# Optimization experiments

Hardware: AMD Instinct MI355X
Metric: run time of the kernel (lower is better)

Reference implementation:

```python
import jax, jax.numpy as jnp
import numpy as np

B, N, D, W = 4, 4096, 256, 7
K = 2 * W + 1  # 15 taps: positions [i-2w, ..., i]
H = 4 * D
EPS = 1e-5


def layer_norm(x, g, b):
    mu = jnp.mean(x, axis=-1, keepdims=True)
    var = jnp.mean(jnp.square(x - mu), axis=-1, keepdims=True)
    return (x - mu) * jax.lax.rsqrt(var + EPS) * g + b


def setup_inputs() -> dict:
    key = jax.random.key(0)
    ks = jax.random.split(key, 8)
    s = 0.02
    return {
        "x": jax.random.normal(ks[0], (B, N, D), dtype=jnp.float32),
        # w_mix[k] is the DxD block of the (K*D -> D) Linear acting on offset k-2w
        "w_mix": (jax.random.normal(ks[1], (K, D, D), dtype=jnp.float32) * s),
        "b_mix": jnp.zeros((D,), dtype=jnp.float32),
        "g1": jnp.ones((D,), jnp.float32) + 0.1 * jax.random.normal(ks[2], (D,), jnp.float32),
        "b1": 0.1 * jax.random.normal(ks[3], (D,), jnp.float32),
        "w_ff1": jax.random.normal(ks[4], (D, H), dtype=jnp.float32) * s,
        "b_ff1": jnp.zeros((H,), dtype=jnp.float32),
        "w_ff2": jax.random.normal(ks[5], (H, D), dtype=jnp.float32) * s,
        "b_ff2": jnp.zeros((D,), dtype=jnp.float32),
        "g2": jnp.ones((D,), jnp.float32) + 0.1 * jax.random.normal(ks[6], (D,), jnp.float32),
        "b2": 0.1 * jax.random.normal(ks[7], (D,), jnp.float32),
    }


def reference(x, w_mix, b_mix, g1, b1, w_ff1, b_ff1, w_ff2, b_ff2, g2, b2):
    # Causal windowed concat + Linear == causal 1D conv with kernel K=2w+1.
    # torch feats chunk k holds x[i - 2w + k]; conv tap k with left pad 2w
    # sees exactly x[i - 2w + k], so kernel = mix weight reshaped (K, D, D).
    mix = jax.lax.conv_general_dilated(
        x, w_mix, window_strides=(1,), padding=[(2 * W, 0)],
        dimension_numbers=("NWC", "WIO", "NWC"),
    ) + b_mix  # [B, N, D]
    # Dropout is identity in eval mode (reference baseline).
    h = layer_norm(x + mix, g1, b1)
    ff = jnp.dot(jax.nn.gelu(jnp.dot(h, w_ff1) + b_ff1, approximate=False), w_ff2) + b_ff2
    return layer_norm(h + ff, g2, b2)
```

## Files before the change

### kernel.cpp

```cpp
#include <hip/hip_runtime.h>
#include <cstdint>

#define DD     256
#define HH     1024
#define NNSEQ  4096
#define KDIM   3840
#define MT     64
#define XROWS  78
#define XPITCH 264
#define APITCH 520
#define FPITCH 260
#define EPSLN  1e-5f

typedef unsigned short u16;
typedef __attribute__((ext_vector_type(8))) short short8;
typedef __attribute__((ext_vector_type(4))) float f32x4;

#define MFMA(a, b, c) __builtin_amdgcn_mfma_f32_16x16x32_bf16(a, b, c, 0, 0, 0)

__device__ __forceinline__ u16 f2bf(float f) {
  unsigned u = __float_as_uint(f);
  u += 0x7FFF + ((u >> 16) & 1);
  return (u16)(u >> 16);
}
__device__ __forceinline__ float bf2f(u16 s) { return __uint_as_float(((unsigned)s) << 16); }

__global__ __launch_bounds__(256) void k_prep(
    const float* __restrict__ wmix, const float* __restrict__ wff1,
    const float* __restrict__ wff2, u16* __restrict__ wpk,
    u16* __restrict__ w1pk, u16* __restrict__ w2pk)
{
  __shared__ float t[32][257];
  const int b = blockIdx.x, tid = threadIdx.x;

  u16* dst;
  if (b < 120) {
    dst = wpk + (size_t)b * 8192;
    for (int r = 0; r < 32; ++r)
      t[r][tid] = wmix[(size_t)(b * 32 + r) * 256 + tid];
  } else if (b < 152) {
    const int u = b - 120, c2 = u >> 3, s = u & 7;
    dst = w1pk + (size_t)u * 8192;
    for (int r = 0; r < 32; ++r)
      t[r][tid] = wff1[(size_t)(s * 32 + r) * 1024 + c2 * 256 + tid];
  } else {
    const int u = b - 152, c2 = u >> 3, s = u & 7;
    dst = w2pk + (size_t)u * 8192;
    for (int r = 0; r < 32; ++r)
      t[r][tid] = wff2[(size_t)(c2 * 256 + s * 32 + r) * 256 + tid];
  }
  __syncthreads();

  const int l = tid & 63, q = l >> 4, cl = l & 15;
#pragma unroll
  for (int f = 0; f < 4; ++f) {
    const int fi = f * 4 + (tid >> 6);
    const int n = fi * 16 + cl;
    uint4 pk;
    unsigned* p = (unsigned*)&pk;
#pragma unroll
    for (int jj = 0; jj < 4; ++jj)
      p[jj] = (unsigned)f2bf(t[q * 8 + jj * 2][n]) | ((unsigned)f2bf(t[q * 8 + jj * 2 + 1][n]) << 16);
    *(uint4*)&dst[(size_t)fi * 512 + l * 8] = pk;
  }
}

__global__ __launch_bounds__(512) void k_conv(
    const float* __restrict__ x, const u16* __restrict__ wpk,
    const float* __restrict__ bmix, u16* __restrict__ yb)
{
  __shared__ u16 xs[XROWS * XPITCH];

  const int tid = threadIdx.x;
  const int wv = tid >> 6, l = tid & 63, q = l >> 4, cl = l & 15;
  const int mg = wv >> 2, ng = wv & 3;
  const int mtile = blockIdx.x >> 2, nb = blockIdx.x & 3;
  const long tok0 = (long)mtile * MT;
  const int n0 = (int)(tok0 & (NNSEQ - 1));

  {
    const int cslot = (tid & 63) * 4;
    for (int r = tid >> 6; r < XROWS; r += 8) {
      const int nloc = n0 - 14 + r;
      float4 v = make_float4(0.f, 0.f, 0.f, 0.f);
      if (nloc >= 0) v = *(const float4*)&x[(tok0 - 14 + r) * DD + cslot];
      uint2 pk;
      pk.x = (unsigned)f2bf(v.x) | ((unsigned)f2bf(v.y) << 16);
      pk.y = (unsigned)f2bf(v.z) | ((unsigned)f2bf(v.w) << 16);
      *(uint2*)&xs[r * XPITCH + cslot] = pk;
    }
  }
  __syncthreads();

  f32x4 acc[4];
  {
    const float bm = (mg == 0) ? bmix[nb * 64 + ng * 16 + cl] : 0.f;
#pragma unroll
    for (int mt = 0; mt < 4; ++mt) acc[mt] = (f32x4){bm, bm, bm, bm};
  }

  const u16* bbase = wpk + (size_t)(mg * 60) * 8192 + (size_t)(nb * 4 + ng) * 512 + (size_t)l * 8;

#define LOAD_A(dst, s_)                                                         \
  {                                                                             \
    const int ks = mg * 60 + (s_);                                              \
    const int xrow = ks >> 3, c0 = (ks & 7) * 32;                               \
    _Pragma("unroll")                                                           \
    for (int mt = 0; mt < 4; ++mt)                                              \
      dst[mt] = *(const short8*)&xs[(xrow + mt * 16 + cl) * XPITCH + c0 + q * 8]; \
  }
#define LOAD_B(dst, s_) dst = *(const short8*)(bbase + (size_t)(s_) * 8192);

  {
    short8 af[4][4], bfr[4];
    LOAD_A(af[0], 0) LOAD_B(bfr[0], 0)
    LOAD_A(af[1], 1) LOAD_B(bfr[1], 1)
    LOAD_A(af[2], 2) LOAD_B(bfr[2], 2)
    LOAD_A(af[3], 3) LOAD_B(bfr[3], 3)

#pragma unroll 4
    for (int s = 0; s < 60; ++s) {
      const int cur = s & 3;
#pragma unroll
      for (int mt = 0; mt < 4; ++mt)
        acc[mt] = MFMA(af[cur][mt], bfr[cur], acc[mt]);
      if (s + 4 < 60) {
        LOAD_A(af[cur], s + 4)
        LOAD_B(bfr[cur], s + 4)
      }
    }
  }
#undef LOAD_A
#undef LOAD_B

  __syncthreads();
  float* rbuf = (float*)xs;
  if (mg == 1) {
#pragma unroll
    for (int mt = 0; mt < 4; ++mt)
#pragma unroll
      for (int reg = 0; reg < 4; ++reg)
        rbuf[(mt * 16 + q * 4 + reg) * 65 + ng * 16 + cl] = acc[mt][reg];
  }
  __syncthreads();

  if (mg == 0) {
#pragma unroll
    for (int mt = 0; mt < 4; ++mt)
#pragma unroll
      for (int reg = 0; reg < 4; ++reg) {
        const int row = mt * 16 + q * 4 + reg;
        const int col = nb * 64 + ng * 16 + cl;
        const float y = acc[mt][reg] + rbuf[row * 65 + ng * 16 + cl]
                      + x[(tok0 + row) * DD + col];
        yb[(tok0 + row) * DD + col] = f2bf(y);
      }
  }
}

__global__ __launch_bounds__(512) void k_ffn(
    const u16* __restrict__ yb, const float* __restrict__ g1,
    const float* __restrict__ b1, const u16* __restrict__ w1pk,
    const float* __restrict__ bf1, const u16* __restrict__ w2pk,
    const float* __restrict__ bf2, const float* __restrict__ g2,
    const float* __restrict__ b2, float* __restrict__ out)
{
  __shared__ u16 hs[64 * XPITCH];
  __shared__ u16 asb[64 * APITCH];
  __shared__ float redS[4][64], redS2[4][64];
  __shared__ float muL[64], invL[64];

  const int tid = threadIdx.x;
  const int wv = tid >> 6, l = tid & 63, q = l >> 4, cl = l & 15;
  const int mg = wv >> 2, ng = wv & 3;
  const long tok0 = (long)blockIdx.x * MT;

  {
    const int chunk = tid & 31;
#pragma unroll
    for (int i = 0; i < 4; ++i) {
      const int row = (tid >> 5) + i * 16;
      *(uint4*)&hs[row * XPITCH + chunk * 8] = *(const uint4*)&yb[(tok0 + row) * DD + chunk * 8];
    }
  }
  __syncthreads();

  {
    const int row = tid >> 3, seg = tid & 7;
    uint4 v[4];
#pragma unroll
    for (int i = 0; i < 4; ++i)
      v[i] = *(const uint4*)&hs[row * XPITCH + seg * 32 + i * 8];
    float yv[32];
#pragma unroll
    for (int i = 0; i < 4; ++i) {
      const unsigned* w = (const unsigned*)&v[i];
#pragma unroll
      for (int j = 0; j < 4; ++j) {
        yv[i * 8 + j * 2]     = __uint_as_float(w[j] << 16);
        yv[i * 8 + j * 2 + 1] = __uint_as_float(w[j] & 0xffff0000u);
      }
    }
    float s = 0.f, s2 = 0.f;
#pragma unroll
    for (int k = 0; k < 32; ++k) { s += yv[k]; s2 += yv[k] * yv[k]; }
#pragma unroll
    for (int off = 1; off < 8; off <<= 1) { s += __shfl_xor(s, off, 64); s2 += __shfl_xor(s2, off, 64); }
    const float mu  = s * (1.f / DD);
    const float var = s2 * (1.f / DD) - mu * mu;
    const float inv = rsqrtf(var + EPSLN);
#pragma unroll
    for (int i = 0; i < 4; ++i) {
      const float4 gv0 = *(const float4*)&g1[seg * 32 + i * 8];
      const float4 gv1 = *(const float4*)&g1[seg * 32 + i * 8 + 4];
      const float4 bv0 = *(const float4*)&b1[seg * 32 + i * 8];
      const float4 bv1 = *(const float4*)&b1[seg * 32 + i * 8 + 4];
      const float g[8] = {gv0.x, gv0.y, gv0.z, gv0.w, gv1.x, gv1.y, gv1.z, gv1.w};
      const float bb[8] = {bv0.x, bv0.y, bv0.z, bv0.w, bv1.x, bv1.y, bv1.z, bv1.w};
      uint4 pk;
      unsigned* p = (unsigned*)&pk;
#pragma unroll
      for (int j = 0; j < 4; ++j) {
        const float h0 = (yv[i * 8 + j * 2]     - mu) * inv * g[j * 2]     + bb[j * 2];
        const float h1 = (yv[i * 8 + j * 2 + 1] - mu) * inv * g[j * 2 + 1] + bb[j * 2 + 1];
        p[j] = (unsigned)f2bf(h0) | ((unsigned)f2bf(h1) << 16);
      }
      *(uint4*)&hs[row * XPITCH + seg * 32 + i * 8] = pk;
    }
  }
  __syncthreads();

  f32x4 acc2[4][4];
#pragma unroll
  for (int nt = 0; nt < 4; ++nt) {
    const float bv = (mg == 0) ? bf2[ng * 64 + nt * 16 + cl] : 0.f;
#pragma unroll
    for (int mt = 0; mt < 4; ++mt) acc2[mt][nt] = (f32x4){bv, bv, bv, bv};
  }

  for (int c = 0; c < 2; ++c) {
    f32x4 acc1[4][4];
#pragma unroll
    for (int nt = 0; nt < 4; ++nt) {
      const float bv = bf1[c * 512 + wv * 64 + nt * 16 + cl];
#pragma unroll
      for (int mt = 0; mt < 4; ++mt) acc1[mt][nt] = (f32x4){bv, bv, bv, bv};
    }
#pragma unroll
    for (int s = 0; s < 8; ++s) {
      short8 a[4], b[4];
#pragma unroll
      for (int mt = 0; mt < 4; ++mt)
        a[mt] = *(const short8*)&hs[(mt * 16 + cl) * XPITCH + s * 32 + q * 8];
      const u16* bp = w1pk + (size_t)((c * 2 + mg) * 8 + s) * 8192 + (size_t)(ng * 4) * 512 + (size_t)l * 8;
#pragma unroll
      for (int nt = 0; nt < 4; ++nt)
        b[nt] = *(const short8*)(bp + nt * 512);
#pragma unroll
      for (int mt = 0; mt < 4; ++mt)
#pragma unroll
        for (int nt = 0; nt < 4; ++nt)
          acc1[mt][nt] = MFMA(a[mt], b[nt], acc1[mt][nt]);
    }
#pragma unroll
    for (int mt = 0; mt < 4; ++mt)
#pragma unroll
      for (int nt = 0; nt < 4; ++nt)
#pragma unroll
        for (int reg = 0; reg < 4; ++reg) {
          const float v = acc1[mt][nt][reg];
          const float g = 0.5f * v * (1.f + erff(v * 0.70710678118654752f));
          asb[(mt * 16 + q * 4 + reg) * APITCH + wv * 64 + nt * 16 + cl] = f2bf(g);
        }
    __syncthreads();
#pragma unroll
    for (int s = 0; s < 8; ++s) {
      short8 a[4], b[4];
#pragma unroll
      for (int mt = 0; mt < 4; ++mt)
        a[mt] = *(const short8*)&asb[(mt * 16 + cl) * APITCH + mg * 256 + s * 32 + q * 8];
      const u16* bp = w2pk + (size_t)((c * 2 + mg) * 8 + s) * 8192 + (size_t)(ng * 4) * 512 + (size_t)l * 8;
#pragma unroll
      for (int nt = 0; nt < 4; ++nt)
        b[nt] = *(const short8*)(bp + nt * 512);
#pragma unroll
      for (int mt = 0; mt < 4; ++mt)
#pragma unroll
        for (int nt = 0; nt < 4; ++nt)
          acc2[mt][nt] = MFMA(a[mt], b[nt], acc2[mt][nt]);
    }
    __syncthreads();
  }

  float* fbuf = (float*)asb;
  if (mg == 1) {
#pragma unroll
    for (int mt = 0; mt < 4; ++mt)
#pragma unroll
      for (int nt = 0; nt < 4; ++nt)
#pragma unroll
        for (int reg = 0; reg < 4; ++reg)
          fbuf[(mt * 16 + q * 4 + reg) * FPITCH + ng * 64 + nt * 16 + cl] = acc2[mt][nt][reg];
  }
  __syncthreads();

  if (mg == 0) {
    float ps[4][4], ps2[4][4];
#pragma unroll
    for (int mt = 0; mt < 4; ++mt)
#pragma unroll
      for (int reg = 0; reg < 4; ++reg) {
        const int row = mt * 16 + q * 4 + reg;
        float s = 0.f, s2 = 0.f;
#pragma unroll
        for (int nt = 0; nt < 4; ++nt) {
          const int col = ng * 64 + nt * 16 + cl;
          float y = acc2[mt][nt][reg] + fbuf[row * FPITCH + col] + bf2f(hs[row * XPITCH + col]);
          acc2[mt][nt][reg] = y;
          s += y; s2 += y * y;
        }
#pragma unroll
        for (int off = 1; off < 16; off <<= 1) { s += __shfl_xor(s, off, 64); s2 += __shfl_xor(s2, off, 64); }
        ps[mt][reg] = s; ps2[mt][reg] = s2;
      }
    if (cl == 0) {
#pragma unroll
      for (int mt = 0; mt < 4; ++mt)
#pragma unroll
        for (int reg = 0; reg < 4; ++reg) {
          const int row = mt * 16 + q * 4 + reg;
          redS[ng][row] = ps[mt][reg]; redS2[ng][row] = ps2[mt][reg];
        }
    }
  }
  __syncthreads();
  if (tid < 64) {
    const float s  = redS[0][tid] + redS[1][tid] + redS[2][tid] + redS[3][tid];
    const float s2 = redS2[0][tid] + redS2[1][tid] + redS2[2][tid] + redS2[3][tid];
    const float mu = s * (1.f / DD);
    const float var = s2 * (1.f / DD) - mu * mu;
    muL[tid] = mu; invL[tid] = rsqrtf(var + EPSLN);
  }
  __syncthreads();

  if (mg == 0) {
#pragma unroll
    for (int nt = 0; nt < 4; ++nt) {
      const int col = ng * 64 + nt * 16 + cl;
      const float gv = g2[col], bv = b2[col];
#pragma unroll
      for (int mt = 0; mt < 4; ++mt)
#pragma unroll
        for (int reg = 0; reg < 4; ++reg) {
          const int row = mt * 16 + q * 4 + reg;
          out[(tok0 + row) * DD + col] = (acc2[mt][nt][reg] - muL[row]) * invL[row] * gv + bv;
        }
    }
  }
}

extern "C" void kernel_launch(void* const* d_in, const int* in_sizes, int n_in,
                              void* d_out, int out_size, void* d_ws, size_t ws_size,
                              hipStream_t stream) {
  const float* x    = (const float*)d_in[0];
  const float* wmix = (const float*)d_in[1];
  const float* bmix = (const float*)d_in[2];
  const float* g1   = (const float*)d_in[3];
  const float* b1   = (const float*)d_in[4];
  const float* wff1 = (const float*)d_in[5];
  const float* bff1 = (const float*)d_in[6];
  const float* wff2 = (const float*)d_in[7];
  const float* bff2 = (const float*)d_in[8];
  const float* g2   = (const float*)d_in[9];
  const float* b2   = (const float*)d_in[10];
  float* out = (float*)d_out;

  u16* wpk  = (u16*)d_ws;
  u16* w1pk = wpk + 983040;
  u16* w2pk = w1pk + 262144;
  u16* yb   = w2pk + 262144;

  k_prep<<<184, 256, 0, stream>>>(wmix, wff1, wff2, wpk, w1pk, w2pk);

  k_conv<<<1024, 512, 0, stream>>>(x, wpk, bmix, yb);
  k_ffn <<<256, 512, 0, stream>>>(yb, g1, b1, w1pk, bff1, w2pk, bff2, g2, b2, out);
}
```

Baseline: 165.6 us.

## Restructure conv and FFN warp tiling to cut split-K reductions and boost reuse

The conv kernel drops from 512 to 256 threads. Each wave now computes a full 64x64 output tile over a quarter of the K dimension, so each loaded A fragment is reused across 4 N-tiles. The split-K partial sums are then combined through a staged tree reduction in shared memory. The FFN kernel changes from a split-K over wave groups to an M-split (each half of the waves owns 32 rows over the full hidden dimension in 4 chunks), which removes the final cross-group reduction buffer and shrinks the activation buffer. This trades fewer redundant loads and reductions for more accumulator registers per wave and more sync stages.

Result: slower. 179.2 us (+8.2%).

```diff
diff --git a/kernel.cpp b/kernel.cpp
--- a/kernel.cpp
+++ b/kernel.cpp
@@ -8,8 +8,6 @@
 #define MT     64
 #define XROWS  78
 #define XPITCH 264
-#define APITCH 520
-#define FPITCH 260
 #define EPSLN  1e-5f
 
 typedef unsigned short u16;
@@ -65,22 +63,22 @@
   }
 }
 
-__global__ __launch_bounds__(512) void k_conv(
+__global__ __launch_bounds__(256, 3) void k_conv(
     const float* __restrict__ x, const u16* __restrict__ wpk,
     const float* __restrict__ bmix, u16* __restrict__ yb)
 {
-  __shared__ u16 xs[XROWS * XPITCH];
+  __shared__ char smem[49920];
+  u16* xs = (u16*)smem;
 
   const int tid = threadIdx.x;
   const int wv = tid >> 6, l = tid & 63, q = l >> 4, cl = l & 15;
-  const int mg = wv >> 2, ng = wv & 3;
   const int mtile = blockIdx.x >> 2, nb = blockIdx.x & 3;
   const long tok0 = (long)mtile * MT;
   const int n0 = (int)(tok0 & (NNSEQ - 1));
 
   {
     const int cslot = (tid & 63) * 4;
-    for (int r = tid >> 6; r < XROWS; r += 8) {
+    for (int r = tid >> 6; r < XROWS; r += 4) {
       const int nloc = n0 - 14 + r;
       float4 v = make_float4(0.f, 0.f, 0.f, 0.f);
       if (nloc >= 0) v = *(const float4*)&x[(tok0 - 14 + r) * DD + cslot];
@@ -92,41 +90,48 @@
   }
   __syncthreads();
 
-  f32x4 acc[4];
-  {
-    const float bm = (mg == 0) ? bmix[nb * 64 + ng * 16 + cl] : 0.f;
-#pragma unroll
-    for (int mt = 0; mt < 4; ++mt) acc[mt] = (f32x4){bm, bm, bm, bm};
-  }
-
-  const u16* bbase = wpk + (size_t)(mg * 60) * 8192 + (size_t)(nb * 4 + ng) * 512 + (size_t)l * 8;
+  f32x4 acc[4][4];
+#pragma unroll
+  for (int nt = 0; nt < 4; ++nt) {
+    const float bm = (wv == 0) ? bmix[nb * 64 + nt * 16 + cl] : 0.f;
+#pragma unroll
+    for (int mt = 0; mt < 4; ++mt) acc[mt][nt] = (f32x4){bm, bm, bm, bm};
+  }
+
+  const u16* bbase = wpk + (size_t)(wv * 30) * 8192 + (size_t)(nb * 4) * 512 + (size_t)l * 8;
 
 #define LOAD_A(dst, s_)                                                         \
   {                                                                             \
-    const int ks = mg * 60 + (s_);                                              \
+    const int ks = wv * 30 + (s_);                                              \
     const int xrow = ks >> 3, c0 = (ks & 7) * 32;                               \
     _Pragma("unroll")                                                           \
     for (int mt = 0; mt < 4; ++mt)                                              \
       dst[mt] = *(const short8*)&xs[(xrow + mt * 16 + cl) * XPITCH + c0 + q * 8]; \
   }
-#define LOAD_B(dst, s_) dst = *(const short8*)(bbase + (size_t)(s_) * 8192);
-
-  {
-    short8 af[4][4], bfr[4];
+#define LOAD_B(dst, s_)                                                         \
+  {                                                                             \
+    const u16* bp = bbase + (size_t)(s_) * 8192;                                \
+    _Pragma("unroll")                                                           \
+    for (int nt = 0; nt < 4; ++nt)                                              \
+      dst[nt] = *(const short8*)(bp + nt * 512);                                \
+  }
+
+  {
+    short8 af[2][4], bfr[2][4];
     LOAD_A(af[0], 0) LOAD_B(bfr[0], 0)
     LOAD_A(af[1], 1) LOAD_B(bfr[1], 1)
-    LOAD_A(af[2], 2) LOAD_B(bfr[2], 2)
-    LOAD_A(af[3], 3) LOAD_B(bfr[3], 3)
-
-#pragma unroll 4
-    for (int s = 0; s < 60; ++s) {
-      const int cur = s & 3;
+
+#pragma unroll 2
+    for (int s = 0; s < 30; ++s) {
+      const int cur = s & 1;
 #pragma unroll
       for (int mt = 0; mt < 4; ++mt)
-        acc[mt] = MFMA(af[cur][mt], bfr[cur], acc[mt]);
-      if (s + 4 < 60) {
-        LOAD_A(af[cur], s + 4)
-        LOAD_B(bfr[cur], s + 4)
+#pragma unroll
+        for (int nt = 0; nt < 4; ++nt)
+          acc[mt][nt] = MFMA(af[cur][mt], bfr[cur][nt], acc[mt][nt]);
+      if (s + 2 < 30) {
+        LOAD_A(af[cur], s + 2)
+        LOAD_B(bfr[cur], s + 2)
       }
     }
   }
@@ -134,28 +139,45 @@
 #undef LOAD_B
 
   __syncthreads();
-  float* rbuf = (float*)xs;
-  if (mg == 1) {
+  float* fb = (float*)smem;
+#define SLOT_W(si)                                                              \
+  _Pragma("unroll")                                                             \
+  for (int mt = 0; mt < 4; ++mt)                                                \
+    _Pragma("unroll")                                                           \
+    for (int nt = 0; nt < 4; ++nt)                                              \
+      _Pragma("unroll")                                                         \
+      for (int reg = 0; reg < 4; ++reg)                                         \
+        fb[(si) * 4160 + (mt * 16 + q * 4 + reg) * 65 + nt * 16 + cl] = acc[mt][nt][reg];
+#define SLOT_R(si)                                                              \
+  _Pragma("unroll")                                                             \
+  for (int mt = 0; mt < 4; ++mt)                                                \
+    _Pragma("unroll")                                                           \
+    for (int nt = 0; nt < 4; ++nt)                                              \
+      _Pragma("unroll")                                                         \
+      for (int reg = 0; reg < 4; ++reg)                                         \
+        acc[mt][nt][reg] += fb[(si) * 4160 + (mt * 16 + q * 4 + reg) * 65 + nt * 16 + cl];
+
+  if (wv == 2) { SLOT_W(0) } else if (wv == 3) { SLOT_W(1) }
+  __syncthreads();
+  if (wv == 0) { SLOT_R(0) } else if (wv == 1) { SLOT_R(1) SLOT_W(2) }
+  __syncthreads();
+  if (wv == 0) {
+    SLOT_R(2)
 #pragma unroll
     for (int mt = 0; mt < 4; ++mt)
 #pragma unroll
-      for (int reg = 0; reg < 4; ++reg)
-        rbuf[(mt * 16 + q * 4 + reg) * 65 + ng * 16 + cl] = acc[mt][reg];
-  }
-  __syncthreads();
-
-  if (mg == 0) {
-#pragma unroll
-    for (int mt = 0; mt < 4; ++mt)
-#pragma unroll
-      for (int reg = 0; reg < 4; ++reg) {
-        const int row = mt * 16 + q * 4 + reg;
-        const int col = nb * 64 + ng * 16 + cl;
-        const float y = acc[mt][reg] + rbuf[row * 65 + ng * 16 + cl]
-                      + x[(tok0 + row) * DD + col];
-        yb[(tok0 + row) * DD + col] = f2bf(y);
-      }
-  }
+      for (int nt = 0; nt < 4; ++nt) {
+        const int col = nb * 64 + nt * 16 + cl;
+#pragma unroll
+        for (int reg = 0; reg < 4; ++reg) {
+          const int row = mt * 16 + q * 4 + reg;
+          const float y = acc[mt][nt][reg] + x[(tok0 + row) * DD + col];
+          yb[(tok0 + row) * DD + col] = f2bf(y);
+        }
+      }
+  }
+#undef SLOT_W
+#undef SLOT_R
 }
 
 __global__ __launch_bounds__(512) void k_ffn(
@@ -166,13 +188,13 @@
     const float* __restrict__ b2, float* __restrict__ out)
 {
   __shared__ u16 hs[64 * XPITCH];
-  __shared__ u16 asb[64 * APITCH];
+  __shared__ u16 asb[64 * XPITCH];
   __shared__ float redS[4][64], redS2[4][64];
   __shared__ float muL[64], invL[64];
 
   const int tid = threadIdx.x;
   const int wv = tid >> 6, l = tid & 63, q = l >> 4, cl = l & 15;
-  const int mg = wv >> 2, ng = wv & 3;
+  const int mh = wv >> 2, ng = wv & 3;
   const long tok0 = (long)blockIdx.x * MT;
 
   {
@@ -230,61 +252,61 @@
   }
   __syncthreads();
 
-  f32x4 acc2[4][4];
+  f32x4 acc2[2][4];
 #pragma unroll
   for (int nt = 0; nt < 4; ++nt) {
-    const float bv = (mg == 0) ? bf2[ng * 64 + nt * 16 + cl] : 0.f;
-#pragma unroll
-    for (int mt = 0; mt < 4; ++mt) acc2[mt][nt] = (f32x4){bv, bv, bv, bv};
-  }
-
-  for (int c = 0; c < 2; ++c) {
-    f32x4 acc1[4][4];
+    const float bv = bf2[ng * 64 + nt * 16 + cl];
+#pragma unroll
+    for (int mt = 0; mt < 2; ++mt) acc2[mt][nt] = (f32x4){bv, bv, bv, bv};
+  }
+
+  for (int c = 0; c < 4; ++c) {
+    f32x4 acc1[2][4];
 #pragma unroll
     for (int nt = 0; nt < 4; ++nt) {
-      const float bv = bf1[c * 512 + wv * 64 + nt * 16 + cl];
-#pragma unroll
-      for (int mt = 0; mt < 4; ++mt) acc1[mt][nt] = (f32x4){bv, bv, bv, bv};
+      const float bv = bf1[c * 256 + ng * 64 + nt * 16 + cl];
+#pragma unroll
+      for (int mt = 0; mt < 2; ++mt) acc1[mt][nt] = (f32x4){bv, bv, bv, bv};
     }
 #pragma unroll
     for (int s = 0; s < 8; ++s) {
-      short8 a[4], b[4];
-#pragma unroll
-      for (int mt = 0; mt < 4; ++mt)
-        a[mt] = *(const short8*)&hs[(mt * 16 + cl) * XPITCH + s * 32 + q * 8];
-      const u16* bp = w1pk + (size_t)((c * 2 + mg) * 8 + s) * 8192 + (size_t)(ng * 4) * 512 + (size_t)l * 8;
+      short8 a[2], b[4];
+#pragma unroll
+      for (int mt = 0; mt < 2; ++mt)
+        a[mt] = *(const short8*)&hs[(mh * 32 + mt * 16 + cl) * XPITCH + s * 32 + q * 8];
+      const u16* bp = w1pk + (size_t)(c * 8 + s) * 8192 + (size_t)(ng * 4) * 512 + (size_t)l * 8;
 #pragma unroll
       for (int nt = 0; nt < 4; ++nt)
         b[nt] = *(const short8*)(bp + nt * 512);
 #pragma unroll
-      for (int mt = 0; mt < 4; ++mt)
+      for (int mt = 0; mt < 2; ++mt)
 #pragma unroll
         for (int nt = 0; nt < 4; ++nt)
           acc1[mt][nt] = MFMA(a[mt], b[nt], acc1[mt][nt]);
     }
 #pragma unroll
-    for (int mt = 0; mt < 4; ++mt)
+    for (int mt = 0; mt < 2; ++mt)
 #pragma unroll
       for (int nt = 0; nt < 4; ++nt)
 #pragma unroll
         for (int reg = 0; reg < 4; ++reg) {
           const float v = acc1[mt][nt][reg];
           const float g = 0.5f * v * (1.f + erff(v * 0.70710678118654752f));
-          asb[(mt * 16 + q * 4 + reg) * APITCH + wv * 64 + nt * 16 + cl] = f2bf(g);
+          asb[(mh * 32 + mt * 16 + q * 4 + reg) * XPITCH + ng * 64 + nt * 16 + cl] = f2bf(g);
         }
     __syncthreads();
 #pragma unroll
     for (int s = 0; s < 8; ++s) {
-      short8 a[4], b[4];
-#pragma unroll
-      for (int mt = 0; mt < 4; ++mt)
-        a[mt] = *(const short8*)&asb[(mt * 16 + cl) * APITCH + mg * 256 + s * 32 + q * 8];
-      const u16* bp = w2pk + (size_t)((c * 2 + mg) * 8 + s) * 8192 + (size_t)(ng * 4) * 512 + (size_t)l * 8;
+      short8 a[2], b[4];
+#pragma unroll
+      for (int mt = 0; mt < 2; ++mt)
+        a[mt] = *(const short8*)&asb[(mh * 32 + mt * 16 + cl) * XPITCH + s * 32 + q * 8];
+      const u16* bp = w2pk + (size_t)(c * 8 + s) * 8192 + (size_t)(ng * 4) * 512 + (size_t)l * 8;
 #pragma unroll
       for (int nt = 0; nt < 4; ++nt)
         b[nt] = *(const short8*)(bp + nt * 512);
 #pragma unroll
-      for (int mt = 0; mt < 4; ++mt)
+      for (int mt = 0; mt < 2; ++mt)
 #pragma unroll
         for (int nt = 0; nt < 4; ++nt)
           acc2[mt][nt] = MFMA(a[mt], b[nt], acc2[mt][nt]);
@@ -292,30 +314,18 @@
     __syncthreads();
   }
 
-  float* fbuf = (float*)asb;
-  if (mg == 1) {
-#pragma unroll
-    for (int mt = 0; mt < 4; ++mt)
-#pragma unroll
-      for (int nt = 0; nt < 4; ++nt)
-#pragma unroll
-        for (int reg = 0; reg < 4; ++reg)
-          fbuf[(mt * 16 + q * 4 + reg) * FPITCH + ng * 64 + nt * 16 + cl] = acc2[mt][nt][reg];
-  }
-  __syncthreads();
-
-  if (mg == 0) {
-    float ps[4][4], ps2[4][4];
-#pragma unroll
-    for (int mt = 0; mt < 4; ++mt)
+  {
+    float ps[2][4], ps2[2][4];
+#pragma unroll
+    for (int mt = 0; mt < 2; ++mt)
 #pragma unroll
       for (int reg = 0; reg < 4; ++reg) {
-        const int row = mt * 16 + q * 4 + reg;
+        const int row = mh * 32 + mt * 16 + q * 4 + reg;
         float s = 0.f, s2 = 0.f;
 #pragma unroll
         for (int nt = 0; nt < 4; ++nt) {
           const int col = ng * 64 + nt * 16 + cl;
-          float y = acc2[mt][nt][reg] + fbuf[row * FPITCH + col] + bf2f(hs[row * XPITCH + col]);
+          const float y = acc2[mt][nt][reg] + bf2f(hs[row * XPITCH + col]);
           acc2[mt][nt][reg] = y;
           s += y; s2 += y * y;
         }
@@ -325,10 +335,10 @@
       }
     if (cl == 0) {
 #pragma unroll
-      for (int mt = 0; mt < 4; ++mt)
+      for (int mt = 0; mt < 2; ++mt)
 #pragma unroll
         for (int reg = 0; reg < 4; ++reg) {
-          const int row = mt * 16 + q * 4 + reg;
+          const int row = mh * 32 + mt * 16 + q * 4 + reg;
           redS[ng][row] = ps[mt][reg]; redS2[ng][row] = ps2[mt][reg];
         }
     }
@@ -343,19 +353,17 @@
   }
   __syncthreads();
 
-  if (mg == 0) {
-#pragma unroll
-    for (int nt = 0; nt < 4; ++nt) {
-      const int col = ng * 64 + nt * 16 + cl;
-      const float gv = g2[col], bv = b2[col];
-#pragma unroll
-      for (int mt = 0; mt < 4; ++mt)
-#pragma unroll
-        for (int reg = 0; reg < 4; ++reg) {
-          const int row = mt * 16 + q * 4 + reg;
-          out[(tok0 + row) * DD + col] = (acc2[mt][nt][reg] - muL[row]) * invL[row] * gv + bv;
-        }
-    }
+#pragma unroll
+  for (int nt = 0; nt < 4; ++nt) {
+    const int col = ng * 64 + nt * 16 + cl;
+    const float gv = g2[col], bv = b2[col];
+#pragma unroll
+    for (int mt = 0; mt < 2; ++mt)
+#pragma unroll
+      for (int reg = 0; reg < 4; ++reg) {
+        const int row = mh * 32 + mt * 16 + q * 4 + reg;
+        out[(tok0 + row) * DD + col] = (acc2[mt][nt][reg] - muL[row]) * invL[row] * gv + bv;
+      }
   }
 }
 
@@ -382,6 +390,6 @@
 
   k_prep<<<184, 256, 0, stream>>>(wmix, wff1, wff2, wpk, w1pk, w2pk);
 
-  k_conv<<<1024, 512, 0, stream>>>(x, wpk, bmix, yb);
+  k_conv<<<1024, 256, 0, stream>>>(x, wpk, bmix, yb);
   k_ffn <<<256, 512, 0, stream>>>(yb, g1, b1, w1pk, bff1, w2pk, bff2, g2, b2, out);
 }
```
